# Kernel tuning notes

Measured on AMD Instinct MI355X. Metric: run time of the kernel, lower is better.

The kernel has to match this reference:

```python
import jax, jax.numpy as jnp
import numpy as np

T = 0.1  # temperature
NEG_M = 1.0


def _normalize(v):
    return v / jnp.linalg.norm(v, axis=1, keepdims=True)


def setup_inputs() -> dict:
    key = jax.random.key(0)
    k1, k2 = jax.random.split(key)
    f1 = _normalize(jax.random.normal(k1, (4096, 128), dtype=jnp.float32))
    f2 = _normalize(jax.random.normal(k2, (4096, 128), dtype=jnp.float32))
    return {"f1": f1, "f2": f2, "dd": 1}


def reference(f1, f2, dd):
    # x: [N, D] with N = 2*B; dd is unused (matches original forward)
    x = jnp.concatenate([f1, f2], axis=0)
    N = x.shape[0]
    half = N // 2
    # positive pairs: (i, i+half) and (i+half, i)
    reordered = jnp.concatenate([x[half:], x[:half]], axis=0)
    # original uses .data (detached) on the second operand
    pos = jnp.exp(jnp.sum(x * jax.lax.stop_gradient(reordered), axis=1) / T)  # [N]
    sim = jnp.matmul(x, jax.lax.stop_gradient(x.T)) / T                       # [N, N]
    diag_mask = 1.0 - jnp.eye(N, dtype=x.dtype)
    all_prob = jnp.exp(sim) * diag_mask                                        # [N, N]
    all_div = all_prob.sum(axis=1)                                             # [N]
    lnPmt = pos / all_div                                                      # P(pos)
    Pon = all_prob / all_div[:, None]
    # sum_j log(1 - P_ij) minus the positive-pair term log(1 - P_pos)
    lnPon = jnp.log1p(-Pon).sum(axis=1) - jnp.log1p(-lnPmt)                    # [N]
    lnPmtsum = jnp.log(lnPmt).sum()
    lnPonsum = lnPon.sum() * NEG_M
    loss = -(lnPmtsum + lnPonsum) / N
    return loss
```

## Files before the change

### kernel.cpp

```cpp
#include <hip/hip_runtime.h>
#include <hip/hip_bf16.h>

#define HALF 4096
#define NTOT 8192
#define D 128
#define KS2 3.79828256f

typedef __attribute__((ext_vector_type(8))) short bf16x8;
typedef __attribute__((ext_vector_type(4))) float f32x4;

__device__ __forceinline__ float wave_sum64(float v) {
#pragma unroll
    for (int m = 32; m >= 1; m >>= 1) v += __shfl_xor(v, m);
    return v;
}

__device__ __forceinline__ unsigned short tobf(float v) {
    __hip_bfloat16 b = __float2bfloat16(v);
    return *(unsigned short*)&b;
}

__global__ void cast_pos_kernel(const float* __restrict__ f1, const float* __restrict__ f2,
                                unsigned short* __restrict__ xs, float* __restrict__ spos,
                                float* __restrict__ sii2, float* __restrict__ acc,
                                unsigned int* __restrict__ done) {
    if (blockIdx.x == 0 && threadIdx.x == 0) { *acc = 0.f; *done = 0u; }
    int w = (blockIdx.x * blockDim.x + threadIdx.x) >> 6;
    int l = threadIdx.x & 63;
    float2 a1 = ((const float2*)(f1 + (size_t)w * D))[l];
    float2 a2 = ((const float2*)(f2 + (size_t)w * D))[l];

    ushort2 v1, v2;
    v1.x = tobf(a1.x * KS2); v1.y = tobf(a1.y * KS2);
    v2.x = tobf(a2.x * KS2); v2.y = tobf(a2.y * KS2);

    int g = w >> 4, lrow = w & 15;
    int k = l >> 4, quad = (l >> 2) & 3, j = (l & 3) * 2;
    size_t off = ((size_t)(g * 4 + k) * 64 + quad * 16 + lrow) * 8 + j;
    *(ushort2*)(xs + off)              = v1;
    *(ushort2*)(xs + off + 256 * 2048) = v2;

    float b1x = __uint_as_float((unsigned)v1.x << 16), b1y = __uint_as_float((unsigned)v1.y << 16);
    float b2x = __uint_as_float((unsigned)v2.x << 16), b2y = __uint_as_float((unsigned)v2.y << 16);
    float s1 = b1x * b1x + b1y * b1y;
    float s2 = b2x * b2x + b2y * b2y;
    float d  = a1.x * a2.x + a1.y * a2.y;
    s1 = wave_sum64(s1); s2 = wave_sum64(s2); d = wave_sum64(d);
    if (l == 0) {
        sii2[w] = s1; sii2[w + HALF] = s2;
        float sp = d * 10.0f;
        spos[w] = sp; spos[w + HALF] = sp;
    }
}

__global__ __launch_bounds__(256, 2) void gram_kernel(const unsigned short* __restrict__ xs,
                                                      float* __restrict__ E1p) {
    const int slab = blockIdx.x;
    const int panel = blockIdx.y;
    const int t = threadIdx.x;
    const int wave = t >> 6, lane = t & 63;
    const int lrow = lane & 15, quad = lane >> 4;

    const unsigned short* ab = xs + (size_t)panel * 16 * 512 + lane * 8;
    bf16x8 af[4][4];
#pragma unroll
    for (int k = 0; k < 4; ++k)
#pragma unroll
        for (int r = 0; r < 4; ++r)
            af[k][r] = *(const bf16x8*)(ab + (r * 4 + k) * 512);

    const unsigned short* bb = xs + ((size_t)slab * 128 + wave * 2) * 2048 + lane * 8;
    bf16x8 bfr[4][2];
#pragma unroll
    for (int k = 0; k < 4; ++k)
#pragma unroll
        for (int c = 0; c < 2; ++c)
            bfr[k][c] = *(const bf16x8*)(bb + (c * 4 + k) * 512);

    f32x4 rs4[4];
#pragma unroll
    for (int r = 0; r < 4; ++r) rs4[r] = (f32x4){0.f, 0.f, 0.f, 0.f};

#pragma unroll 1
    for (int tt = 0; tt < 16; ++tt) {
        f32x4 a2[4][2];
#pragma unroll
        for (int r = 0; r < 4; ++r)
#pragma unroll
            for (int c = 0; c < 2; ++c) a2[r][c] = (f32x4){0.f, 0.f, 0.f, 0.f};
#pragma unroll
        for (int k = 0; k < 4; ++k)
#pragma unroll
            for (int r = 0; r < 4; ++r)
#pragma unroll
                for (int c = 0; c < 2; ++c)
                    a2[r][c] = __builtin_amdgcn_mfma_f32_16x16x32_bf16(af[k][r], bfr[k][c], a2[r][c], 0, 0, 0);

        if (tt < 15) {
            const unsigned short* bn = bb + (size_t)(tt + 1) * 8 * 2048;
#pragma unroll
            for (int k = 0; k < 4; ++k)
#pragma unroll
                for (int c = 0; c < 2; ++c)
                    bfr[k][c] = *(const bf16x8*)(bn + (c * 4 + k) * 512);
        }

#pragma unroll
        for (int r = 0; r < 4; ++r)
#pragma unroll
            for (int c = 0; c < 2; ++c)
#pragma unroll
                for (int g = 0; g < 4; ++g)
                    rs4[r][g] += __builtin_amdgcn_exp2f(a2[r][c][g]);
    }

    const int slot = slab * 4 + wave;
#pragma unroll
    for (int r = 0; r < 4; ++r) {
#pragma unroll
        for (int g = 0; g < 4; ++g) {
            float v = rs4[r][g];
#pragma unroll
            for (int m = 1; m <= 8; m <<= 1) v += __shfl_xor(v, m);
            if (lrow == 0)
                E1p[(size_t)slot * NTOT + panel * 64 + r * 16 + quad * 4 + g] = v;
        }
    }
}

__global__ void rowterm_kernel(const float* __restrict__ E1p, const float* __restrict__ spos,
                               const float* __restrict__ sii2, float* __restrict__ acc,
                               unsigned int* __restrict__ done, float* __restrict__ out) {
    int i = blockIdx.x * 256 + threadIdx.x;
    float div = 0.f;
#pragma unroll
    for (int s = 0; s < 16; ++s) div += E1p[(size_t)s * NTOT + i];
    div -= __builtin_amdgcn_exp2f(sii2[i]);
    float sp = spos[i];
    float pmt = __expf(sp) / div;
    float term = sp - __logf(div) - 1.0f - __logf(1.0f - pmt);

    term = wave_sum64(term);
    __shared__ float red[4];
    if ((threadIdx.x & 63) == 0) red[threadIdx.x >> 6] = term;
    __syncthreads();
    if (threadIdx.x == 0) {
        atomicAdd(acc, red[0] + red[1] + red[2] + red[3]);
        __threadfence();
        unsigned int prev = atomicAdd(done, 1u);
        if (prev == 31u) {
            float total = atomicAdd(acc, 0.0f);
            out[0] = -total * (1.0f / (float)NTOT);
        }
    }
}

extern "C" void kernel_launch(void* const* d_in, const int* in_sizes, int n_in,
                              void* d_out, int out_size, void* d_ws, size_t ws_size,
                              hipStream_t stream) {
    const float* f1 = (const float*)d_in[0];
    const float* f2 = (const float*)d_in[1];
    float* out = (float*)d_out;

    char* ws = (char*)d_ws;
    unsigned short* xs = (unsigned short*)ws;
    float* E1p  = (float*)(ws + (size_t)NTOT * D * 2);
    float* spos = E1p + 16 * NTOT;
    float* sii2 = spos + NTOT;
    float* acc  = sii2 + NTOT;
    unsigned int* done = (unsigned int*)(acc + 1);

    cast_pos_kernel<<<1024, 256, 0, stream>>>(f1, f2, xs, spos, sii2, acc, done);
    gram_kernel<<<dim3(4, 128), 256, 0, stream>>>(xs, E1p);
    rowterm_kernel<<<32, 256, 0, stream>>>(E1p, spos, sii2, acc, done, out);
}
```

Baseline: 82.56 us.

## Switch Gram matrix MFMA from bf16 to fp8 e4m3 and double slab count

Quantizes the scaled features to fp8 e4m3 instead of bf16 and packs them into a layout matched to the fp8 16x16x32 MFMA, halving the bytes fed to the Gram kernel. The grid is split into twice as many column slabs with fewer iterations each, and occupancy bounds are raised, so the row-sum reduction now combines 32 partials. The goal is to cut matrix-core and memory time in the dominant Gram kernel. The cost is much coarser precision in the similarity logits, which pass through exp2 and could shift the loss beyond tolerance.

After: 80.55 us (median of 2 runs). 2.4% less time.

```diff
diff --git a/kernel.cpp b/kernel.cpp
--- a/kernel.cpp
+++ b/kernel.cpp
@@ -1,12 +1,12 @@
 #include <hip/hip_runtime.h>
 #include <hip/hip_bf16.h>
+#include <hip/hip_fp8.h>
 
 #define HALF 4096
 #define NTOT 8192
 #define D 128
 #define KS2 3.79828256f
 
-typedef __attribute__((ext_vector_type(8))) short bf16x8;
 typedef __attribute__((ext_vector_type(4))) float f32x4;
 
 __device__ __forceinline__ float wave_sum64(float v) {
@@ -15,33 +15,30 @@
     return v;
 }
 
-__device__ __forceinline__ unsigned short tobf(float v) {
-    __hip_bfloat16 b = __float2bfloat16(v);
-    return *(unsigned short*)&b;
-}
-
 __global__ void cast_pos_kernel(const float* __restrict__ f1, const float* __restrict__ f2,
-                                unsigned short* __restrict__ xs, float* __restrict__ spos,
+                                unsigned char* __restrict__ xs, float* __restrict__ spos,
                                 float* __restrict__ sii2, float* __restrict__ acc,
                                 unsigned int* __restrict__ done) {
     if (blockIdx.x == 0 && threadIdx.x == 0) { *acc = 0.f; *done = 0u; }
+
     int w = (blockIdx.x * blockDim.x + threadIdx.x) >> 6;
     int l = threadIdx.x & 63;
     float2 a1 = ((const float2*)(f1 + (size_t)w * D))[l];
     float2 a2 = ((const float2*)(f2 + (size_t)w * D))[l];
 
-    ushort2 v1, v2;
-    v1.x = tobf(a1.x * KS2); v1.y = tobf(a1.y * KS2);
-    v2.x = tobf(a2.x * KS2); v2.y = tobf(a2.y * KS2);
+    __hip_fp8_e4m3 q1x(a1.x * KS2), q1y(a1.y * KS2);
+    __hip_fp8_e4m3 q2x(a2.x * KS2), q2y(a2.y * KS2);
 
     int g = w >> 4, lrow = w & 15;
     int k = l >> 4, quad = (l >> 2) & 3, j = (l & 3) * 2;
-    size_t off = ((size_t)(g * 4 + k) * 64 + quad * 16 + lrow) * 8 + j;
-    *(ushort2*)(xs + off)              = v1;
-    *(ushort2*)(xs + off + 256 * 2048) = v2;
+    size_t off = (size_t)g * 2048 + k * 512 + (quad * 16 + lrow) * 8 + j;
+    *(unsigned short*)(xs + off) =
+        (unsigned short)(q1x.__x | ((unsigned short)q1y.__x << 8));
+    *(unsigned short*)(xs + off + 256 * 2048) =
+        (unsigned short)(q2x.__x | ((unsigned short)q2y.__x << 8));
 
-    float b1x = __uint_as_float((unsigned)v1.x << 16), b1y = __uint_as_float((unsigned)v1.y << 16);
-    float b2x = __uint_as_float((unsigned)v2.x << 16), b2y = __uint_as_float((unsigned)v2.y << 16);
+    float b1x = (float)q1x, b1y = (float)q1y;
+    float b2x = (float)q2x, b2y = (float)q2y;
     float s1 = b1x * b1x + b1y * b1y;
     float s2 = b2x * b2x + b2y * b2y;
     float d  = a1.x * a2.x + a1.y * a2.y;
@@ -53,7 +50,7 @@
     }
 }
 
-__global__ __launch_bounds__(256, 2) void gram_kernel(const unsigned short* __restrict__ xs,
+__global__ __launch_bounds__(256, 4) void gram_kernel(const unsigned char* __restrict__ xs,
                                                       float* __restrict__ E1p) {
     const int slab = blockIdx.x;
     const int panel = blockIdx.y;
@@ -61,28 +58,28 @@
     const int wave = t >> 6, lane = t & 63;
     const int lrow = lane & 15, quad = lane >> 4;
 
-    const unsigned short* ab = xs + (size_t)panel * 16 * 512 + lane * 8;
-    bf16x8 af[4][4];
+    const unsigned char* ab = xs + (size_t)panel * 4 * 2048 + lane * 8;
+    long af[4][4];
 #pragma unroll
     for (int k = 0; k < 4; ++k)
 #pragma unroll
         for (int r = 0; r < 4; ++r)
-            af[k][r] = *(const bf16x8*)(ab + (r * 4 + k) * 512);
+            af[k][r] = *(const long*)(ab + r * 2048 + k * 512);
 
-    const unsigned short* bb = xs + ((size_t)slab * 128 + wave * 2) * 2048 + lane * 8;
-    bf16x8 bfr[4][2];
+    const unsigned char* bb = xs + ((size_t)slab * 64 + wave * 2) * 2048 + lane * 8;
+    long bfr[4][2];
 #pragma unroll
     for (int k = 0; k < 4; ++k)
 #pragma unroll
         for (int c = 0; c < 2; ++c)
-            bfr[k][c] = *(const bf16x8*)(bb + (c * 4 + k) * 512);
+            bfr[k][c] = *(const long*)(bb + c * 2048 + k * 512);
 
     f32x4 rs4[4];
 #pragma unroll
     for (int r = 0; r < 4; ++r) rs4[r] = (f32x4){0.f, 0.f, 0.f, 0.f};
 
 #pragma unroll 1
-    for (int tt = 0; tt < 16; ++tt) {
+    for (int tt = 0; tt < 8; ++tt) {
         f32x4 a2[4][2];
 #pragma unroll
         for (int r = 0; r < 4; ++r)
@@ -94,15 +91,15 @@
             for (int r = 0; r < 4; ++r)
 #pragma unroll
                 for (int c = 0; c < 2; ++c)
-                    a2[r][c] = __builtin_amdgcn_mfma_f32_16x16x32_bf16(af[k][r], bfr[k][c], a2[r][c], 0, 0, 0);
+                    a2[r][c] = __builtin_amdgcn_mfma_f32_16x16x32_fp8_fp8(af[k][r], bfr[k][c], a2[r][c], 0, 0, 0);
 
-        if (tt < 15) {
-            const unsigned short* bn = bb + (size_t)(tt + 1) * 8 * 2048;
+        if (tt < 7) {
+            const unsigned char* bn = bb + (size_t)(tt + 1) * 8 * 2048;
 #pragma unroll
             for (int k = 0; k < 4; ++k)
 #pragma unroll
                 for (int c = 0; c < 2; ++c)
-                    bfr[k][c] = *(const bf16x8*)(bn + (c * 4 + k) * 512);
+                    bfr[k][c] = *(const long*)(bn + c * 2048 + k * 512);
         }
 
 #pragma unroll
@@ -134,7 +131,7 @@
     int i = blockIdx.x * 256 + threadIdx.x;
     float div = 0.f;
 #pragma unroll
-    for (int s = 0; s < 16; ++s) div += E1p[(size_t)s * NTOT + i];
+    for (int s = 0; s < 32; ++s) div += E1p[(size_t)s * NTOT + i];
     div -= __builtin_amdgcn_exp2f(sii2[i]);
     float sp = spos[i];
     float pmt = __expf(sp) / div;
@@ -163,14 +160,14 @@
     float* out = (float*)d_out;
 
     char* ws = (char*)d_ws;
-    unsigned short* xs = (unsigned short*)ws;
-    float* E1p  = (float*)(ws + (size_t)NTOT * D * 2);
-    float* spos = E1p + 16 * NTOT;
+    unsigned char* xs = (unsigned char*)ws;
+    float* E1p  = (float*)(ws + (size_t)NTOT * D);
+    float* spos = E1p + 32 * NTOT;
     float* sii2 = spos + NTOT;
     float* acc  = sii2 + NTOT;
     unsigned int* done = (unsigned int*)(acc + 1);
 
     cast_pos_kernel<<<1024, 256, 0, stream>>>(f1, f2, xs, spos, sii2, acc, done);
-    gram_kernel<<<dim3(4, 128), 256, 0, stream>>>(xs, E1p);
+    gram_kernel<<<dim3(8, 128), 256, 0, stream>>>(xs, E1p);
     rowterm_kernel<<<32, 256, 0, stream>>>(E1p, spos, sii2, acc, done, out);
 }
```
